# Performance work log

Hardware: AMD Instinct MI355X
Metric: run time of the kernel (lower is better)

The kernel has to match this reference:

```python
import jax, jax.numpy as jnp
import numpy as np

B, D, L = 32, 576, 196          # batch, literals per patch, patches
Cc, K = 10, 256                 # classes, clauses per class
M = Cc * K                      # total clauses
MASK_DENSITY = 0.02             # fraction of literals included per clause (sparse so clauses actually fire)


def setup_inputs() -> dict:
    key = jax.random.key(0)
    k1, k2, k3 = jax.random.split(key, 3)
    # literals in {0,1} as float (as produced by the upstream TMCNNClass binarizer)
    literals = jax.random.bernoulli(k1, 0.5, (B, D, L)).astype(jnp.float32)
    # sparse clause selection masks [M, D]
    clause_mask = jax.random.uniform(k2, (M, D)) < MASK_DENSITY
    # per-clause vote weights alpha [M]
    alpha = jax.random.normal(k3, (M,), dtype=jnp.float32)
    return {"literals": literals, "clause_mask": clause_mask, "alpha": alpha}


def reference(literals, clause_mask, alpha):
    # Original: lit_masked = where(mask, lit, 1); clause_map = lit_masked.min(dim=D) == 1.
    # With literals in {0,1} this AND-reduce equals: no selected literal is 0, i.e.
    # sum over selected literals of (1 - lit) == 0. Expressed as a GEMM to avoid
    # materializing the B*M*D*L broadcast intermediate.
    mask_f = clause_mask.astype(literals.dtype)                 # [M, D]
    miss = jnp.einsum('md,bdl->bml', mask_f, 1.0 - literals)    # [B, M, L] count of violated literals
    clause_map = miss < 0.5                                     # exact ==0 test on small nonneg ints
    clause_or = jnp.any(clause_map, axis=-1)                    # [B, M] OR over patches

    # Weighted vote: first K/2 clauses per class are positive, second K/2 negative.
    z = clause_or.astype(literals.dtype).reshape(B, Cc, K)      # [B, Cc, K]
    h = K // 2
    sign = jnp.concatenate([jnp.ones((h,), literals.dtype), -jnp.ones((h,), literals.dtype)])
    logits = jnp.einsum('bck,ck->bc', z, alpha.reshape(Cc, K) * sign)  # [B, Cc]
    return clause_map, clause_or, logits
```

## Files before the change

kernel.cpp:

```cpp
#include <hip/hip_runtime.h>
#include <stdint.h>

#define B  32
#define D  576
#define L  196
#define CC 10
#define K  256
#define M  (CC * K)
#define SLOTS 64
#define NF4 49
#define MT 64

#define PACK_BLOCKS ((B * D + 3) / 4)
#define CSR_BLOCKS  ((M + 3) / 4)

__global__ __launch_bounds__(256) void prologue_k(
    const float* __restrict__ lit, const int* __restrict__ mask,
    uint64_t* __restrict__ litbits, int* __restrict__ cnt,
    uint16_t* __restrict__ list) {
    const int lane = threadIdx.x & 63;
    const int wave = threadIdx.x >> 6;

    if (blockIdx.x < PACK_BLOCKS) {
        const int wid = blockIdx.x * 4 + wave;
        if (wid >= B * D) return;
        const int b = wid % B;
        const int d = wid / B;
        const float* base = lit + ((size_t)b * D + d) * L;

        uint64_t w0 = __ballot(base[lane] > 0.5f);
        uint64_t w1 = __ballot(base[64 + lane] > 0.5f);
        uint64_t w2 = __ballot(base[128 + lane] > 0.5f);
        float tail = (lane < 4) ? base[192 + lane] : 0.0f;
        uint64_t w3 = __ballot(tail > 0.5f);

        uint64_t* out = litbits + ((size_t)b * D + d) * 4;
        if (lane == 0) { out[0] = w0; out[1] = w1; out[2] = w2; out[3] = w3; }
    } else {
        const int m = (blockIdx.x - PACK_BLOCKS) * 4 + wave;
        if (m >= M) return;
        const int* row = mask + (size_t)m * D;
        int base = 0;
#pragma unroll
        for (int r = 0; r < 9; ++r) {
            int d = r * 64 + lane;
            bool sel = (row[d] != 0);
            uint64_t bal = __ballot(sel);
            if (sel) {
                int pos = base + __popcll(bal & ((1ull << lane) - 1ull));
                if (pos < SLOTS) list[(size_t)m * SLOTS + pos] = (uint16_t)d;
            }
            base += __popcll(bal);
        }
        if (lane == 0) cnt[m] = (base < SLOTS) ? base : SLOTS;
    }
}

__global__ __launch_bounds__(256) void clause_eval5_k(
    const uint64_t* __restrict__ litbits, const int* __restrict__ cnt,
    const uint16_t* __restrict__ list, float* __restrict__ cmap,
    float* __restrict__ cor) {
    __shared__ uint64_t lit_s[D * 4];
    __shared__ uint16_t listT[SLOTS * MT];
    __shared__ uint64_t res[MT * 4];
    __shared__ int      sh_cnt[MT];

    const int t  = threadIdx.x;
    const int m0 = blockIdx.x * MT;
    const int b  = blockIdx.y;

    {
        const uint4* gp = (const uint4*)(litbits + (size_t)b * D * 4);
        uint4* sp = (uint4*)lit_s;
#pragma unroll
        for (int i = 0; i < 4; ++i) sp[t + 256 * i] = gp[t + 256 * i];
        if (t < D * 2 - 1024) sp[1024 + t] = gp[1024 + t];
    }
    {
        const uint4* lp = (const uint4*)(list + (size_t)m0 * SLOTS);
#pragma unroll
        for (int i = 0; i < 2; ++i) {
            int idx = t + 256 * i;
            uint4 v = lp[idx];
            const uint16_t* e = (const uint16_t*)&v;
            int c  = idx >> 3;
            int s0 = (idx & 7) * 8;
#pragma unroll
            for (int j = 0; j < 8; ++j) listT[(s0 + j) * MT + c] = e[j];
        }
        if (t < MT) sh_cnt[t] = cnt[m0 + t];
    }
    __syncthreads();

    {
        const int c = t >> 2;
        const int h = t & 3;
        const int n = sh_cnt[c];
        uint64_t a = ~0ull;
        for (int k = 0; k < n; ++k) {
            int d = (int)listT[k * MT + c];
            a &= lit_s[d * 4 + h];
        }
        res[t] = a;
    }
    __syncthreads();

    {
        float4* outp = (float4*)cmap + ((size_t)b * M + m0) * NF4;
        for (int f = t; f < MT * NF4; f += 256) {
            int c  = f / NF4;
            int q  = f - c * NF4;
            int wd = q >> 4;
            int sh = (q & 15) * 4;
            unsigned nib = (unsigned)((res[c * 4 + wd] >> sh) & 0xFull);
            float4 o;
            o.x = (nib & 1u) ? 1.0f : 0.0f;
            o.y = (nib & 2u) ? 1.0f : 0.0f;
            o.z = (nib & 4u) ? 1.0f : 0.0f;
            o.w = (nib & 8u) ? 1.0f : 0.0f;
            outp[f] = o;
        }
    }

    if (t < MT) {
        uint64_t w = res[t * 4] | res[t * 4 + 1] | res[t * 4 + 2] |
                     (res[t * 4 + 3] & 0xFull);
        cor[(size_t)b * M + m0 + t] = w ? 1.0f : 0.0f;
    }
}

__global__ __launch_bounds__(256) void logits_k(
    const float* __restrict__ cor, const float* __restrict__ alpha,
    float* __restrict__ logits) {
    const int c = blockIdx.x % CC;
    const int b = blockIdx.x / CC;
    const int k = threadIdx.x;
    const float sgn = (k < (K / 2)) ? 1.0f : -1.0f;
    float v = cor[(size_t)b * M + (size_t)c * K + k] * alpha[(size_t)c * K + k] * sgn;
#pragma unroll
    for (int off = 32; off > 0; off >>= 1) v += __shfl_down(v, off, 64);
    __shared__ float sv[4];
    if ((k & 63) == 0) sv[k >> 6] = v;
    __syncthreads();
    if (k == 0) logits[blockIdx.x] = sv[0] + sv[1] + sv[2] + sv[3];
}

extern "C" void kernel_launch(void* const* d_in, const int* in_sizes, int n_in,
                              void* d_out, int out_size, void* d_ws, size_t ws_size,
                              hipStream_t stream) {
    const float* lit   = (const float*)d_in[0];
    const int*   mask  = (const int*)  d_in[1];
    const float* alpha = (const float*)d_in[2];

    float* out    = (float*)d_out;
    float* cmap   = out;
    float* cor    = out + (size_t)B * M * L;
    float* logits = cor + (size_t)B * M;

    uint64_t* litbits = (uint64_t*)d_ws;
    int*      cnt     = (int*)(litbits + (size_t)B * D * 4);
    uint16_t* list    = (uint16_t*)(cnt + M);

    prologue_k<<<PACK_BLOCKS + CSR_BLOCKS, 256, 0, stream>>>(
        lit, mask, litbits, cnt, list);

    clause_eval5_k<<<dim3(M / MT, B), 256, 0, stream>>>(
        litbits, cnt, list, cmap, cor);

    logits_k<<<B * CC, 256, 0, stream>>>(cor, alpha, logits);
}
```

Before: 101.5 us.

## Fuse three kernels into one cooperative kernel with grid-wide syncs

Merges the pack/CSR prologue, clause evaluation and logits reduction into a single cooperative kernel launched with a fixed grid of 1280 blocks, separated by grid.sync barriers. The aim is to remove the launch overhead and inter-kernel gaps of three separate launches. The trade-offs are grid barrier costs, an occupancy hint requiring five blocks per CU to fit all blocks co-resident, and shared memory allocated during phases that don't use it.

```diff
diff --git a/kernel.cpp b/kernel.cpp
--- a/kernel.cpp
+++ b/kernel.cpp
@@ -1,5 +1,8 @@
 #include <hip/hip_runtime.h>
+#include <hip/hip_cooperative_groups.h>
 #include <stdint.h>
+
+namespace cg = cooperative_groups;
 
 #define B  32
 #define D  576
@@ -10,20 +13,26 @@
 #define SLOTS 64
 #define NF4 49
 #define MT 64
+#define GRID 1280
 
-#define PACK_BLOCKS ((B * D + 3) / 4)
-#define CSR_BLOCKS  ((M + 3) / 4)
+__global__ __launch_bounds__(256, 5) void tm_fused_k(
+    const float* __restrict__ lit, const int* __restrict__ mask,
+    const float* __restrict__ alpha, uint64_t* __restrict__ litbits,
+    int* __restrict__ cnt, uint16_t* __restrict__ list,
+    float* __restrict__ cmap, float* __restrict__ cor,
+    float* __restrict__ logits) {
+    cg::grid_group grid = cg::this_grid();
 
-__global__ __launch_bounds__(256) void prologue_k(
-    const float* __restrict__ lit, const int* __restrict__ mask,
-    uint64_t* __restrict__ litbits, int* __restrict__ cnt,
-    uint16_t* __restrict__ list) {
-    const int lane = threadIdx.x & 63;
-    const int wave = threadIdx.x >> 6;
+    __shared__ uint64_t lit_s[D * 4];
+    __shared__ uint16_t listT[SLOTS * MT];
+    __shared__ uint64_t res[MT * 4];
+    __shared__ int      sh_cnt[MT];
 
-    if (blockIdx.x < PACK_BLOCKS) {
-        const int wid = blockIdx.x * 4 + wave;
-        if (wid >= B * D) return;
+    const int t    = threadIdx.x;
+    const int lane = t & 63;
+    const int wave = t >> 6;
+
+    for (int wid = blockIdx.x * 4 + wave; wid < B * D; wid += GRID * 4) {
         const int b = wid % B;
         const int d = wid / B;
         const float* base = lit + ((size_t)b * D + d) * L;
@@ -36,9 +45,9 @@
 
         uint64_t* out = litbits + ((size_t)b * D + d) * 4;
         if (lane == 0) { out[0] = w0; out[1] = w1; out[2] = w2; out[3] = w3; }
-    } else {
-        const int m = (blockIdx.x - PACK_BLOCKS) * 4 + wave;
-        if (m >= M) return;
+    }
+    if (wave < 2) {
+        const int m = blockIdx.x * 2 + wave;
         const int* row = mask + (size_t)m * D;
         int base = 0;
 #pragma unroll
@@ -54,20 +63,11 @@
         }
         if (lane == 0) cnt[m] = (base < SLOTS) ? base : SLOTS;
     }
-}
 
-__global__ __launch_bounds__(256) void clause_eval5_k(
-    const uint64_t* __restrict__ litbits, const int* __restrict__ cnt,
-    const uint16_t* __restrict__ list, float* __restrict__ cmap,
-    float* __restrict__ cor) {
-    __shared__ uint64_t lit_s[D * 4];
-    __shared__ uint16_t listT[SLOTS * MT];
-    __shared__ uint64_t res[MT * 4];
-    __shared__ int      sh_cnt[MT];
+    grid.sync();
 
-    const int t  = threadIdx.x;
-    const int m0 = blockIdx.x * MT;
-    const int b  = blockIdx.y;
+    const int m0 = (blockIdx.x % (M / MT)) * MT;
+    const int b  = blockIdx.x / (M / MT);
 
     {
         const uint4* gp = (const uint4*)(litbits + (size_t)b * D * 4);
@@ -127,22 +127,23 @@
                      (res[t * 4 + 3] & 0xFull);
         cor[(size_t)b * M + m0 + t] = w ? 1.0f : 0.0f;
     }
-}
 
-__global__ __launch_bounds__(256) void logits_k(
-    const float* __restrict__ cor, const float* __restrict__ alpha,
-    float* __restrict__ logits) {
-    const int c = blockIdx.x % CC;
-    const int b = blockIdx.x / CC;
-    const int k = threadIdx.x;
-    const float sgn = (k < (K / 2)) ? 1.0f : -1.0f;
-    float v = cor[(size_t)b * M + (size_t)c * K + k] * alpha[(size_t)c * K + k] * sgn;
+    grid.sync();
+
+    if (blockIdx.x < B * CC) {
+        const int c = blockIdx.x % CC;
+        const int bb = blockIdx.x / CC;
+        const int k = t;
+        const float sgn = (k < (K / 2)) ? 1.0f : -1.0f;
+        float v = cor[(size_t)bb * M + (size_t)c * K + k] *
+                  alpha[(size_t)c * K + k] * sgn;
 #pragma unroll
-    for (int off = 32; off > 0; off >>= 1) v += __shfl_down(v, off, 64);
-    __shared__ float sv[4];
-    if ((k & 63) == 0) sv[k >> 6] = v;
-    __syncthreads();
-    if (k == 0) logits[blockIdx.x] = sv[0] + sv[1] + sv[2] + sv[3];
+        for (int off = 32; off > 0; off >>= 1) v += __shfl_down(v, off, 64);
+        __shared__ float sv[4];
+        if ((k & 63) == 0) sv[k >> 6] = v;
+        __syncthreads();
+        if (k == 0) logits[blockIdx.x] = sv[0] + sv[1] + sv[2] + sv[3];
+    }
 }
 
 extern "C" void kernel_launch(void* const* d_in, const int* in_sizes, int n_in,
@@ -161,11 +162,9 @@
     int*      cnt     = (int*)(litbits + (size_t)B * D * 4);
     uint16_t* list    = (uint16_t*)(cnt + M);
 
-    prologue_k<<<PACK_BLOCKS + CSR_BLOCKS, 256, 0, stream>>>(
-        lit, mask, litbits, cnt, list);
-
-    clause_eval5_k<<<dim3(M / MT, B), 256, 0, stream>>>(
-        litbits, cnt, list, cmap, cor);
-
-    logits_k<<<B * CC, 256, 0, stream>>>(cor, alpha, logits);
+    void* args[] = {(void*)&lit, (void*)&mask, (void*)&alpha,
+                    (void*)&litbits, (void*)&cnt, (void*)&list,
+                    (void*)&cmap, (void*)&cor, (void*)&logits};
+    hipLaunchCooperativeKernel((const void*)tm_fused_k, dim3(GRID), dim3(256),
+                               args, 0, stream);
 }
```

New measurement: 332.5 us. +227.5%, slower.
